# Kernel tuning notes

Measured on AMD Instinct MI355X. Metric: run time of the kernel, lower is better.

Reference implementation:

```python
import jax, jax.numpy as jnp
import numpy as np

NUM_LANDMARKS = 64
INV_ITERS = 6
B, S, D = 32, 8192, 64  # batch*heads, seq_len, head_dim


def landmark_pool(x, n=NUM_LANDMARKS):
    # x: [B, S, D]; S % n == 0 -> mean over contiguous segments of length S//n
    b, s, d = x.shape
    seg = s // n
    return x.reshape(b, n, seg, d).mean(axis=2)  # [B, n, D]


def iterative_pinv(k_mat, n_iter=INV_ITERS):
    # k_mat: [B, m, m] row-stochastic softmax matrix; Razavi Newton-Schulz pinv
    m = k_mat.shape[-1]
    i_mat = jnp.eye(m, dtype=k_mat.dtype)
    # per-batch init: 1 / max_j(sum_i K_ij) * K^T
    col_sums = jnp.sum(k_mat, axis=-2)                      # [B, m]
    init_scale = 1.0 / jnp.max(col_sums, axis=-1)           # [B]
    v = init_scale[:, None, None] * jnp.swapaxes(k_mat, -1, -2)
    for _ in range(n_iter):
        kv = jnp.matmul(k_mat, v)
        v = jnp.matmul(0.25 * v, 13.0 * i_mat - jnp.matmul(kv, 15.0 * i_mat - jnp.matmul(kv, 7.0 * i_mat - kv)))
    return v


def setup_inputs() -> dict:
    key = jax.random.key(0)
    kq, kk, kv = jax.random.split(key, 3)
    q = jax.random.normal(kq, (B, S, D), dtype=jnp.float32)
    k = jax.random.normal(kk, (B, S, D), dtype=jnp.float32)
    v = jax.random.normal(kv, (B, S, D), dtype=jnp.float32)
    return {"q": q, "k": k, "v": v}


def reference(q, k, v):
    d = k.shape[-1]
    scale = 1.0 / jnp.sqrt(jnp.asarray(d, dtype=q.dtype))
    q_land = landmark_pool(q)   # [B, m, D]
    k_land = landmark_pool(k)   # [B, m, D]
    # kernel_1: softmax(q k_land^T / sqrt(d))  -> [B, S, m]
    kernel_1 = jax.nn.softmax(jnp.einsum('bsd,bmd->bsm', q * scale, k_land), axis=-1)
    # kernel_2: softmax(q_land k_land^T / sqrt(d)) -> [B, m, m]
    kernel_2 = jax.nn.softmax(jnp.einsum('bnd,bmd->bnm', q_land * scale, k_land), axis=-1)
    # kernel_3: softmax(q_land k^T / sqrt(d)) @ v -> [B, m, D]
    att_3 = jax.nn.softmax(jnp.einsum('bmd,bsd->bms', q_land * scale, k), axis=-1)
    kernel_3 = jnp.einsum('bms,bsd->bmd', att_3, v)
    kernel_2_inv = iterative_pinv(kernel_2)
    x = jnp.einsum('bsm,bmn->bsn', kernel_1, kernel_2_inv)
    x = jnp.einsum('bsn,bnd->bsd', x, kernel_3)
    return x
```

## Files before the change

### kernel.cpp

```cpp
#include <hip/hip_runtime.h>
#include <math.h>

#define NB 32
#define SLEN 8192
#define DIM 64
#define M 64
#define SEG 128
#define SPLITS 32
#define CHUNK 256


#define ACC16(ax0, ax1, ax2, ax3, bv)                                          \
  c[0][0] = fmaf(ax0, bv.x, c[0][0]); c[0][1] = fmaf(ax0, bv.y, c[0][1]);      \
  c[0][2] = fmaf(ax0, bv.z, c[0][2]); c[0][3] = fmaf(ax0, bv.w, c[0][3]);      \
  c[1][0] = fmaf(ax1, bv.x, c[1][0]); c[1][1] = fmaf(ax1, bv.y, c[1][1]);      \
  c[1][2] = fmaf(ax1, bv.z, c[1][2]); c[1][3] = fmaf(ax1, bv.w, c[1][3]);      \
  c[2][0] = fmaf(ax2, bv.x, c[2][0]); c[2][1] = fmaf(ax2, bv.y, c[2][1]);      \
  c[2][2] = fmaf(ax2, bv.z, c[2][2]); c[2][3] = fmaf(ax2, bv.w, c[2][3]);      \
  c[3][0] = fmaf(ax3, bv.x, c[3][0]); c[3][1] = fmaf(ax3, bv.y, c[3][1]);      \
  c[3][2] = fmaf(ax3, bv.z, c[3][2]); c[3][3] = fmaf(ax3, bv.w, c[3][3]);

__device__ __forceinline__ void mm_p1(const float* A, int lda, const float* B,
                                      int ldb, int r0, int n0, float (&c)[4][4]) {
  #pragma unroll 4
  for (int kk = 0; kk < 64; kk += 4) {
    float4 a0 = *(const float4*)(A + (r0 + 0) * lda + kk);
    float4 a1 = *(const float4*)(A + (r0 + 1) * lda + kk);
    float4 a2 = *(const float4*)(A + (r0 + 2) * lda + kk);
    float4 a3 = *(const float4*)(A + (r0 + 3) * lda + kk);
    float4 b0 = *(const float4*)(B + (kk + 0) * ldb + n0);
    float4 b1 = *(const float4*)(B + (kk + 1) * ldb + n0);
    float4 b2 = *(const float4*)(B + (kk + 2) * ldb + n0);
    float4 b3 = *(const float4*)(B + (kk + 3) * ldb + n0);
    ACC16(a0.x, a1.x, a2.x, a3.x, b0)
    ACC16(a0.y, a1.y, a2.y, a3.y, b1)
    ACC16(a0.z, a1.z, a2.z, a3.z, b2)
    ACC16(a0.w, a1.w, a2.w, a3.w, b3)
  }
}

__device__ __forceinline__ void mm_p1_tf(const float* A, int lda, const float* B,
                                         int ldb, float cd, int r0, int n0,
                                         float (&c)[4][4]) {
  #pragma unroll 4
  for (int kk = 0; kk < 64; kk += 4) {
    float4 a0 = *(const float4*)(A + (r0 + 0) * lda + kk);
    float4 a1 = *(const float4*)(A + (r0 + 1) * lda + kk);
    float4 a2 = *(const float4*)(A + (r0 + 2) * lda + kk);
    float4 a3 = *(const float4*)(A + (r0 + 3) * lda + kk);
    #pragma unroll
    for (int t = 0; t < 4; ++t) {
      float4 bb = *(const float4*)(B + (kk + t) * ldb + n0);
      int r = kk + t;
      bb.x = ((r == n0 + 0) ? cd : 0.f) - bb.x;
      bb.y = ((r == n0 + 1) ? cd : 0.f) - bb.y;
      bb.z = ((r == n0 + 2) ? cd : 0.f) - bb.z;
      bb.w = ((r == n0 + 3) ? cd : 0.f) - bb.w;
      float av0 = (t == 0) ? a0.x : (t == 1) ? a0.y : (t == 2) ? a0.z : a0.w;
      float av1 = (t == 0) ? a1.x : (t == 1) ? a1.y : (t == 2) ? a1.z : a1.w;
      float av2 = (t == 0) ? a2.x : (t == 1) ? a2.y : (t == 2) ? a2.z : a2.w;
      float av3 = (t == 0) ? a3.x : (t == 1) ? a3.y : (t == 2) ? a3.z : a3.w;
      ACC16(av0, av1, av2, av3, bb)
    }
  }
}

__device__ __forceinline__ void mm_p2(const float* A, int lda, const float* B,
                                      int ldb, int m0, int n0, float (&c)[4][4]) {
  #pragma unroll 4
  for (int s = 0; s < 64; ++s) {
    float4 e = *(const float4*)(A + s * lda + m0);
    float4 vv = *(const float4*)(B + s * ldb + n0);
    ACC16(e.x, e.y, e.z, e.w, vv)
  }
}

__global__ __launch_bounds__(256) void pool_kernel(
    const float* __restrict__ q, const float* __restrict__ k,
    float* __restrict__ ql_s, float* __restrict__ kl) {
  int b = blockIdx.x >> 6, n = blockIdx.x & 63;
  int tid = threadIdx.x;
  int rg = tid >> 4, d4 = tid & 15;
  const float* qb = q + ((size_t)b * SLEN + (size_t)n * SEG) * DIM;
  const float* kb = k + ((size_t)b * SLEN + (size_t)n * SEG) * DIM;
  float4 aq = make_float4(0.f, 0.f, 0.f, 0.f);
  float4 ak = make_float4(0.f, 0.f, 0.f, 0.f);
  #pragma unroll
  for (int j = 0; j < 8; ++j) {
    int r = rg * 8 + j;
    float4 t = *(const float4*)(qb + r * DIM + 4 * d4);
    aq.x += t.x; aq.y += t.y; aq.z += t.z; aq.w += t.w;
    float4 u = *(const float4*)(kb + r * DIM + 4 * d4);
    ak.x += u.x; ak.y += u.y; ak.z += u.z; ak.w += u.w;
  }
  __shared__ float4 sq[256], sk[256];
  sq[tid] = aq; sk[tid] = ak;
  __syncthreads();
  #pragma unroll
  for (int off = 128; off >= 16; off >>= 1) {
    if (tid < off) {
      float4 a = sq[tid], bb = sq[tid + off];
      sq[tid] = make_float4(a.x + bb.x, a.y + bb.y, a.z + bb.z, a.w + bb.w);
      float4 c2 = sk[tid], d2 = sk[tid + off];
      sk[tid] = make_float4(c2.x + d2.x, c2.y + d2.y, c2.z + d2.z, c2.w + d2.w);
    }
    __syncthreads();
  }
  if (tid < 16) {
    float4 a = sq[tid], bb = sk[tid];
    size_t o = ((size_t)b * M + n) * DIM + 4 * tid;
    const float qs = 0.125f / 128.f, ks = 1.f / 128.f;
    *(float4*)(ql_s + o) = make_float4(a.x * qs, a.y * qs, a.z * qs, a.w * qs);
    *(float4*)(kl + o) = make_float4(bb.x * ks, bb.y * ks, bb.z * ks, bb.w * ks);
  }
}

__global__ __launch_bounds__(256) void phaseB_pinv_kernel(
    const float* __restrict__ k, const float* __restrict__ v,
    const float* __restrict__ ql_s, const float* __restrict__ klg,
    float* num_p, float* den_p, float* k2inv_g, float* k2_g) {
  __shared__ float smem[13312];
  int tid = threadIdx.x;
  int r0 = (tid >> 4) << 2, c0 = (tid & 15) << 2;

  if (blockIdx.x >= NB) {
    int blk = blockIdx.x - NB;
    int b = blk >> 5, sp = blk & 31;
    float* qlT = smem;
    float* kv = smem + 4352;
    float* Es = smem + 8704;
    float* dredF = smem + 13056;

    #pragma unroll
    for (int i = 0; i < 16; ++i) {
      int e = tid + 256 * i;
      qlT[(e & 63) * 68 + (e >> 6)] = ql_s[(size_t)b * 4096 + e];
    }
    int m_den = tid & 63, qg = tid >> 6;
    float den_acc = 0.f;
    float cN[4][4];
    #pragma unroll
    for (int i = 0; i < 4; ++i)
      #pragma unroll
      for (int j = 0; j < 4; ++j) cN[i][j] = 0.f;

    const float* kbase = k + ((size_t)b * SLEN + (size_t)sp * CHUNK) * DIM;
    const float* vbase = v + ((size_t)b * SLEN + (size_t)sp * CHUNK) * DIM;

    for (int sc = 0; sc < 4; ++sc) {
      #pragma unroll
      for (int i = 0; i < 4; ++i) {
        int idx = tid + 256 * i;
        int s = idx >> 4, j = idx & 15;
        *(float4*)(kv + s * 68 + 4 * j) =
            *(const float4*)(kbase + (size_t)(sc * 64 + s) * DIM + 4 * j);
      }
      __syncthreads();
      float c[4][4];
      #pragma unroll
      for (int i = 0; i < 4; ++i)
        #pragma unroll
        for (int j = 0; j < 4; ++j) c[i][j] = 0.f;
      mm_p1(kv, 68, qlT, 68, r0, c0, c);
      #pragma unroll
      for (int i = 0; i < 4; ++i)
        #pragma unroll
        for (int j = 0; j < 4; ++j) c[i][j] = __expf(c[i][j]);
      __syncthreads();
      #pragma unroll
      for (int i = 0; i < 4; ++i)
        *(float4*)(Es + (r0 + i) * 68 + c0) =
            make_float4(c[i][0], c[i][1], c[i][2], c[i][3]);
      #pragma unroll
      for (int i = 0; i < 4; ++i) {
        int idx = tid + 256 * i;
        int s = idx >> 4, j = idx & 15;
        *(float4*)(kv + s * 68 + 4 * j) =
            *(const float4*)(vbase + (size_t)(sc * 64 + s) * DIM + 4 * j);
      }
      __syncthreads();
      #pragma unroll
      for (int t = 0; t < 16; ++t) den_acc += Es[(qg * 16 + t) * 68 + m_den];
      mm_p2(Es, 68, kv, 68, r0, c0, cN);
      __syncthreads();
    }
    dredF[qg * 64 + m_den] = den_acc;
    __syncthreads();
    if (tid < 64)
      den_p[((size_t)b * SPLITS + sp) * 64 + tid] =
          dredF[tid] + dredF[64 + tid] + dredF[128 + tid] + dredF[192 + tid];
    float* np = num_p + ((size_t)b * SPLITS + sp) * 4096;
    #pragma unroll
    for (int i = 0; i < 4; ++i)
      *(float4*)(np + (size_t)(r0 + i) * 64 + c0) =
          make_float4(cN[i][0], cN[i][1], cN[i][2], cN[i][3]);
  } else {
    int b = blockIdx.x;
    float* b1 = smem;
    float* b2 = smem + 4352;
    float* b3 = smem + 8704;
    float* red = smem + 13056;
    float* k2b = k2_g + (size_t)b * 4096;

    #pragma unroll
    for (int i = 0; i < 4; ++i) {
      int idx = tid + 256 * i;
      int s = idx >> 4, j = idx & 15;
      *(float4*)(b1 + s * 68 + 4 * j) =
          *(const float4*)(ql_s + (size_t)b * 4096 + (size_t)s * 64 + 4 * j);
    }
    #pragma unroll
    for (int i = 0; i < 16; ++i) {
      int e = tid + 256 * i;
      b2[(e & 63) * 68 + (e >> 6)] = klg[(size_t)b * 4096 + e];
    }
    __syncthreads();
    float c[4][4];
    #pragma unroll
    for (int i = 0; i < 4; ++i)
      #pragma unroll
      for (int j = 0; j < 4; ++j) c[i][j] = 0.f;
    mm_p1(b1, 68, b2, 68, r0, c0, c);
    #pragma unroll
    for (int i = 0; i < 4; ++i) {
      float pr = 0.f;
      #pragma unroll
      for (int j = 0; j < 4; ++j) { c[i][j] = __expf(c[i][j]); pr += c[i][j]; }
      b3[(r0 + i) * 16 + (tid & 15)] = pr;
    }
    __syncthreads();
    if (tid < 64) {
      float rs = 0.f;
      #pragma unroll
      for (int g = 0; g < 16; ++g) rs += b3[tid * 16 + g];
      red[tid] = 1.f / rs;
    }
    __syncthreads();
    #pragma unroll
    for (int i = 0; i < 4; ++i) {
      float inv = red[r0 + i];
      #pragma unroll
      for (int j = 0; j < 4; ++j) c[i][j] *= inv;
      float4 val = make_float4(c[i][0], c[i][1], c[i][2], c[i][3]);
      *(float4*)(k2b + (size_t)(r0 + i) * 64 + c0) = val;
      *(float4*)(b3 + (r0 + i) * 68 + c0) = val;
    }
    __syncthreads();
    if (tid < 64) {
      float cs = 0.f;
      #pragma unroll 8
      for (int n2 = 0; n2 < 64; ++n2) cs += b3[n2 * 68 + tid];
      float mx = cs;
      #pragma unroll
      for (int off = 1; off < 64; off <<= 1) mx = fmaxf(mx, __shfl_xor(mx, off));
      red[0] = 1.f / mx;
    }
    __syncthreads();
    float iscale = red[0];
    #pragma unroll
    for (int i = 0; i < 16; ++i) {
      int e = tid + 256 * i;
      int r = e >> 6, cc = e & 63;
      b1[r * 68 + cc] = b3[cc * 68 + r] * iscale;
    }
    __syncthreads();

    for (int it = 0; it < 6; ++it) {
      #pragma unroll
      for (int i = 0; i < 4; ++i)
        #pragma unroll
        for (int j = 0; j < 4; ++j) c[i][j] = 0.f;
      mm_p1(k2b, 64, b1, 68, r0, c0, c);
      #pragma unroll
      for (int i = 0; i < 4; ++i)
        *(float4*)(b2 + (r0 + i) * 68 + c0) =
            make_float4(c[i][0], c[i][1], c[i][2], c[i][3]);
      __syncthreads();
      #pragma unroll
      for (int i = 0; i < 4; ++i)
        #pragma unroll
        for (int j = 0; j < 4; ++j) c[i][j] = 0.f;
      mm_p1_tf(b2, 68, b2, 68, 7.f, r0, c0, c);
      #pragma unroll
      for (int i = 0; i < 4; ++i)
        *(float4*)(b3 + (r0 + i) * 68 + c0) =
            make_float4(c[i][0], c[i][1], c[i][2], c[i][3]);
      __syncthreads();
      #pragma unroll
      for (int i = 0; i < 4; ++i)
        #pragma unroll
        for (int j = 0; j < 4; ++j) c[i][j] = 0.f;
      mm_p1_tf(b2, 68, b3, 68, 15.f, r0, c0, c);
      __syncthreads();
      #pragma unroll
      for (int i = 0; i < 4; ++i)
        *(float4*)(b3 + (r0 + i) * 68 + c0) =
            make_float4(c[i][0], c[i][1], c[i][2], c[i][3]);
      __syncthreads();
      #pragma unroll
      for (int i = 0; i < 4; ++i)
        #pragma unroll
        for (int j = 0; j < 4; ++j) c[i][j] = 0.f;
      mm_p1_tf(b1, 68, b3, 68, 13.f, r0, c0, c);
      __syncthreads();
      #pragma unroll
      for (int i = 0; i < 4; ++i)
        *(float4*)(b1 + (r0 + i) * 68 + c0) = make_float4(
            0.25f * c[i][0], 0.25f * c[i][1], 0.25f * c[i][2], 0.25f * c[i][3]);
      __syncthreads();
    }
    #pragma unroll
    for (int i = 0; i < 16; ++i) {
      int e = tid + 256 * i;
      k2inv_g[(size_t)b * 4096 + e] = b1[(e >> 6) * 68 + (e & 63)];
    }
  }
}

__global__ __launch_bounds__(256) void combine1_kernel(
    const float* __restrict__ num_p, const float* __restrict__ den_p,
    float* __restrict__ k3) {
  int b = blockIdx.x >> 3, slice = blockIdx.x & 7;
  int tid = threadIdx.x;
  int e0 = slice * 512 + tid * 2;
  float a0 = 0.f, a1 = 0.f;
  for (int sp = 0; sp < SPLITS; ++sp) {
    float2 t = *(const float2*)(num_p + ((size_t)b * SPLITS + sp) * 4096 + e0);
    a0 += t.x; a1 += t.y;
  }
  int m = e0 >> 6;
  float dsum = 0.f;
  for (int sp = 0; sp < SPLITS; ++sp)
    dsum += den_p[((size_t)b * SPLITS + sp) * 64 + m];
  float dinv = 1.f / dsum;
  *(float2*)(k3 + (size_t)b * 4096 + e0) = make_float2(a0 * dinv, a1 * dinv);
}

__global__ __launch_bounds__(256) void combine2_kernel(
    const float* __restrict__ k2inv, const float* __restrict__ k3,
    float* __restrict__ Wm) {
  __shared__ float A[4352], Bm[4352];
  int b = blockIdx.x, tid = threadIdx.x;
  int r0 = (tid >> 4) << 2, c0 = (tid & 15) << 2;
  #pragma unroll
  for (int i = 0; i < 4; ++i) {
    int idx = tid + 256 * i;
    int s = idx >> 4, j = idx & 15;
    *(float4*)(A + s * 68 + 4 * j) =
        *(const float4*)(k2inv + (size_t)b * 4096 + (size_t)s * 64 + 4 * j);
    *(float4*)(Bm + s * 68 + 4 * j) =
        *(const float4*)(k3 + (size_t)b * 4096 + (size_t)s * 64 + 4 * j);
  }
  __syncthreads();
  float c[4][4];
  #pragma unroll
  for (int i = 0; i < 4; ++i)
    #pragma unroll
    for (int j = 0; j < 4; ++j) c[i][j] = 0.f;
  mm_p1(A, 68, Bm, 68, r0, c0, c);
  #pragma unroll
  for (int i = 0; i < 4; ++i)
    *(float4*)(Wm + (size_t)b * 4096 + (size_t)(r0 + i) * 64 + c0) =
        make_float4(c[i][0], c[i][1], c[i][2], c[i][3]);
}

#define FROWS 128
__global__ __launch_bounds__(256) void final_kernel(
    const float* __restrict__ q, const float* __restrict__ klg,
    const float* __restrict__ Wm, float* __restrict__ out) {
  __shared__ float smem[13120];
  float* klT = smem;
  float* Wl = smem + 4352;
  float* Es = smem + 8448;
  float* dred = smem + 12800;
  float* denF = smem + 13056;
  int b = blockIdx.x >> 6, rb = blockIdx.x & 63;
  int tid = threadIdx.x;
  int r0 = (tid >> 4) << 2, c0 = (tid & 15) << 2;
  int rr = tid & 63, qg = tid >> 6;

  #pragma unroll
  for (int i = 0; i < 16; ++i) {
    int e = tid + 256 * i;
    klT[(e & 63) * 68 + (e >> 6)] = klg[(size_t)b * 4096 + e];
  }
  #pragma unroll
  for (int i = 0; i < 4; ++i) {
    int idx = tid + 256 * i;
    *(float4*)(Wl + idx * 4) = *(const float4*)(Wm + (size_t)b * 4096 + idx * 4);
  }
  __syncthreads();

  for (int sc = 0; sc < FROWS / 64; ++sc) {
    const float* qsrc = q + ((size_t)b * SLEN + (size_t)rb * FROWS + sc * 64) * DIM;
    #pragma unroll
    for (int i = 0; i < 4; ++i) {
      int idx = tid + 256 * i;
      int s = idx >> 4, j = idx & 15;
      float4 t = *(const float4*)(qsrc + (size_t)s * DIM + 4 * j);
      *(float4*)(Es + s * 68 + 4 * j) =
          make_float4(t.x * 0.125f, t.y * 0.125f, t.z * 0.125f, t.w * 0.125f);
    }
    __syncthreads();
    float c[4][4];
    #pragma unroll
    for (int i = 0; i < 4; ++i)
      #pragma unroll
      for (int j = 0; j < 4; ++j) c[i][j] = 0.f;
    mm_p1(Es, 68, klT, 68, r0, c0, c);
    #pragma unroll
    for (int i = 0; i < 4; ++i)
      #pragma unroll
      for (int j = 0; j < 4; ++j) c[i][j] = __expf(c[i][j]);
    __syncthreads();
    #pragma unroll
    for (int i = 0; i < 4; ++i)
      *(float4*)(Es + (r0 + i) * 68 + c0) =
          make_float4(c[i][0], c[i][1], c[i][2], c[i][3]);
    __syncthreads();
    float ds = 0.f;
    #pragma unroll
    for (int t = 0; t < 4; ++t) {
      float4 x = *(const float4*)(Es + rr * 68 + qg * 16 + 4 * t);
      ds += (x.x + x.y) + (x.z + x.w);
    }
    dred[qg * 64 + rr] = ds;
    __syncthreads();
    if (tid < 64)
      denF[tid] =
          1.f / (dred[tid] + dred[64 + tid] + dred[128 + tid] + dred[192 + tid]);
    __syncthreads();
    float c3[4][4];
    #pragma unroll
    for (int i = 0; i < 4; ++i)
      #pragma unroll
      for (int j = 0; j < 4; ++j) c3[i][j] = 0.f;
    mm_p1(Es, 68, Wl, 64, r0, c0, c3);
    float* orow = out + ((size_t)b * SLEN + (size_t)rb * FROWS + sc * 64) * DIM;
    #pragma unroll
    for (int i = 0; i < 4; ++i) {
      float inv = denF[r0 + i];
      *(float4*)(orow + (size_t)(r0 + i) * 64 + c0) = make_float4(
          c3[i][0] * inv, c3[i][1] * inv, c3[i][2] * inv, c3[i][3] * inv);
    }
    __syncthreads();
  }
}

extern "C" void kernel_launch(void* const* d_in, const int* in_sizes, int n_in,
                              void* d_out, int out_size, void* d_ws, size_t ws_size,
                              hipStream_t stream) {
  (void)in_sizes; (void)n_in; (void)out_size; (void)ws_size;
  const float* q = (const float*)d_in[0];
  const float* k = (const float*)d_in[1];
  const float* v = (const float*)d_in[2];
  float* out = (float*)d_out;
  float* ws = (float*)d_ws;

  float* ql_s = ws;
  float* kl = ws + 131072;
  float* k2inv = ws + 262144;
  float* Wm = ws + 393216;
  float* k3 = ws + 524288;
  float* den_p = ws + 655360;
  float* num_p = ws + 720896;

  pool_kernel<<<NB * 64, 256, 0, stream>>>(q, k, ql_s, kl);
  phaseB_pinv_kernel<<<NB + NB * SPLITS, 256, 0, stream>>>(
      k, v, ql_s, kl, num_p, den_p, k2inv, Wm);
  combine1_kernel<<<NB * 8, 256, 0, stream>>>(num_p, den_p, k3);
  combine2_kernel<<<NB, 256, 0, stream>>>(k2inv, k3, Wm);
  final_kernel<<<NB * 64, 256, 0, stream>>>(q, kl, Wm, out);
}
```

Before: 350.1 us.

## Prefetch tiles into registers, enlarge per-block chunks, shuffle-reduce softmax denominators

The phase-B and final kernels now load the next 64-row tile of k/v or q into registers while the current tile is computed, so global load latency overlaps with the LDS matmuls. Each block handles more rows (chunk 512, 16 splits; final kernel 512 rows per block), which cuts the block count and the redundant per-block setup of landmark and weight tiles. The final kernel computes row-sum denominators with 16-lane shuffles instead of an LDS reduction, removing two barriers per tile. The cost is fewer blocks in flight on a large GPU, extra register pressure from the prefetch buffers, and dependence on combine1 honouring the new SPLITS value.

Measured after the change: 367.3 us. 1.05x slower.

```diff
diff --git a/kernel.cpp b/kernel.cpp
--- a/kernel.cpp
+++ b/kernel.cpp
@@ -6,8 +6,11 @@
 #define DIM 64
 #define M 64
 #define SEG 128
-#define SPLITS 32
-#define CHUNK 256
+#define SPLITS 16
+#define CHUNK 512
+#define TILES 8
+#define FROWS 512
+#define FTILES 8
 
 
 #define ACC16(ax0, ax1, ax2, ax3, bv)                                          \
@@ -75,6 +78,19 @@
   }
 }
 
+__device__ __forceinline__ void load_tile4(float4 (&dst)[4], const float* base,
+                                           int t, int srow, int scol4) {
+  #pragma unroll
+  for (int i = 0; i < 4; ++i)
+    dst[i] = *(const float4*)(base + (size_t)(t * 64 + srow + 16 * i) * DIM + scol4);
+}
+__device__ __forceinline__ void store_tile4(float* lds, const float4 (&src)[4],
+                                            int srow, int scol4) {
+  #pragma unroll
+  for (int i = 0; i < 4; ++i)
+    *(float4*)(lds + (srow + 16 * i) * 68 + scol4) = src[i];
+}
+
 __global__ __launch_bounds__(256) void pool_kernel(
     const float* __restrict__ q, const float* __restrict__ k,
     float* __restrict__ ql_s, float* __restrict__ kl) {
@@ -122,10 +138,11 @@
   __shared__ float smem[13312];
   int tid = threadIdx.x;
   int r0 = (tid >> 4) << 2, c0 = (tid & 15) << 2;
+  int srow = tid >> 4, scol4 = (tid & 15) << 2;
 
   if (blockIdx.x >= NB) {
     int blk = blockIdx.x - NB;
-    int b = blk >> 5, sp = blk & 31;
+    int b = blk >> 4, sp = blk & 15;
     float* qlT = smem;
     float* kv = smem + 4352;
     float* Es = smem + 8704;
@@ -147,14 +164,13 @@
     const float* kbase = k + ((size_t)b * SLEN + (size_t)sp * CHUNK) * DIM;
     const float* vbase = v + ((size_t)b * SLEN + (size_t)sp * CHUNK) * DIM;
 
-    for (int sc = 0; sc < 4; ++sc) {
-      #pragma unroll
-      for (int i = 0; i < 4; ++i) {
-        int idx = tid + 256 * i;
-        int s = idx >> 4, j = idx & 15;
-        *(float4*)(kv + s * 68 + 4 * j) =
-            *(const float4*)(kbase + (size_t)(sc * 64 + s) * DIM + 4 * j);
-      }
+    float4 kreg[4], vreg[4];
+    load_tile4(kreg, kbase, 0, srow, scol4);
+    load_tile4(vreg, vbase, 0, srow, scol4);
+
+    for (int sc = 0; sc < TILES; ++sc) {
+      store_tile4(kv, kreg, srow, scol4);
+      if (sc < TILES - 1) load_tile4(kreg, kbase, sc + 1, srow, scol4);
       __syncthreads();
       float c[4][4];
       #pragma unroll
@@ -167,17 +183,12 @@
         #pragma unroll
         for (int j = 0; j < 4; ++j) c[i][j] = __expf(c[i][j]);
       __syncthreads();
+      store_tile4(kv, vreg, srow, scol4);
       #pragma unroll
       for (int i = 0; i < 4; ++i)
         *(float4*)(Es + (r0 + i) * 68 + c0) =
             make_float4(c[i][0], c[i][1], c[i][2], c[i][3]);
-      #pragma unroll
-      for (int i = 0; i < 4; ++i) {
-        int idx = tid + 256 * i;
-        int s = idx >> 4, j = idx & 15;
-        *(float4*)(kv + s * 68 + 4 * j) =
-            *(const float4*)(vbase + (size_t)(sc * 64 + s) * DIM + 4 * j);
-      }
+      if (sc < TILES - 1) load_tile4(vreg, vbase, sc + 1, srow, scol4);
       __syncthreads();
       #pragma unroll
       for (int t = 0; t < 16; ++t) den_acc += Es[(qg * 16 + t) * 68 + m_den];
@@ -364,20 +375,17 @@
         make_float4(c[i][0], c[i][1], c[i][2], c[i][3]);
 }
 
-#define FROWS 128
 __global__ __launch_bounds__(256) void final_kernel(
     const float* __restrict__ q, const float* __restrict__ klg,
     const float* __restrict__ Wm, float* __restrict__ out) {
-  __shared__ float smem[13120];
+  __shared__ float smem[12800];
   float* klT = smem;
   float* Wl = smem + 4352;
   float* Es = smem + 8448;
-  float* dred = smem + 12800;
-  float* denF = smem + 13056;
-  int b = blockIdx.x >> 6, rb = blockIdx.x & 63;
+  int b = blockIdx.x >> 4, rb = blockIdx.x & 15;
   int tid = threadIdx.x;
   int r0 = (tid >> 4) << 2, c0 = (tid & 15) << 2;
-  int rr = tid & 63, qg = tid >> 6;
+  int srow = tid >> 4, scol4 = (tid & 15) << 2;
 
   #pragma unroll
   for (int i = 0; i < 16; ++i) {
@@ -389,18 +397,20 @@
     int idx = tid + 256 * i;
     *(float4*)(Wl + idx * 4) = *(const float4*)(Wm + (size_t)b * 4096 + idx * 4);
   }
-  __syncthreads();
-
-  for (int sc = 0; sc < FROWS / 64; ++sc) {
-    const float* qsrc = q + ((size_t)b * SLEN + (size_t)rb * FROWS + sc * 64) * DIM;
+
+  const float* qbase = q + ((size_t)b * SLEN + (size_t)rb * FROWS) * DIM;
+  float* obase = out + ((size_t)b * SLEN + (size_t)rb * FROWS) * DIM;
+  float4 qreg[4];
+  load_tile4(qreg, qbase, 0, srow, scol4);
+
+  for (int sc = 0; sc < FTILES; ++sc) {
     #pragma unroll
     for (int i = 0; i < 4; ++i) {
-      int idx = tid + 256 * i;
-      int s = idx >> 4, j = idx & 15;
-      float4 t = *(const float4*)(qsrc + (size_t)s * DIM + 4 * j);
-      *(float4*)(Es + s * 68 + 4 * j) =
+      float4 t = qreg[i];
+      *(float4*)(Es + (srow + 16 * i) * 68 + scol4) =
           make_float4(t.x * 0.125f, t.y * 0.125f, t.z * 0.125f, t.w * 0.125f);
     }
+    if (sc < FTILES - 1) load_tile4(qreg, qbase, sc + 1, srow, scol4);
     __syncthreads();
     float c[4][4];
     #pragma unroll
@@ -412,37 +422,31 @@
     for (int i = 0; i < 4; ++i)
       #pragma unroll
       for (int j = 0; j < 4; ++j) c[i][j] = __expf(c[i][j]);
-    __syncthreads();
+    float inv[4];
+    #pragma unroll
+    for (int i = 0; i < 4; ++i) {
+      float s = (c[i][0] + c[i][1]) + (c[i][2] + c[i][3]);
+      s += __shfl_xor(s, 1);
+      s += __shfl_xor(s, 2);
+      s += __shfl_xor(s, 4);
+      s += __shfl_xor(s, 8);
+      inv[i] = 1.f / s;
+    }
     #pragma unroll
     for (int i = 0; i < 4; ++i)
       *(float4*)(Es + (r0 + i) * 68 + c0) =
           make_float4(c[i][0], c[i][1], c[i][2], c[i][3]);
-    __syncthreads();
-    float ds = 0.f;
-    #pragma unroll
-    for (int t = 0; t < 4; ++t) {
-      float4 x = *(const float4*)(Es + rr * 68 + qg * 16 + 4 * t);
-      ds += (x.x + x.y) + (x.z + x.w);
-    }
-    dred[qg * 64 + rr] = ds;
-    __syncthreads();
-    if (tid < 64)
-      denF[tid] =
-          1.f / (dred[tid] + dred[64 + tid] + dred[128 + tid] + dred[192 + tid]);
-    __syncthreads();
     float c3[4][4];
     #pragma unroll
     for (int i = 0; i < 4; ++i)
       #pragma unroll
       for (int j = 0; j < 4; ++j) c3[i][j] = 0.f;
     mm_p1(Es, 68, Wl, 64, r0, c0, c3);
-    float* orow = out + ((size_t)b * SLEN + (size_t)rb * FROWS + sc * 64) * DIM;
-    #pragma unroll
-    for (int i = 0; i < 4; ++i) {
-      float inv = denF[r0 + i];
-      *(float4*)(orow + (size_t)(r0 + i) * 64 + c0) = make_float4(
-          c3[i][0] * inv, c3[i][1] * inv, c3[i][2] * inv, c3[i][3] * inv);
-    }
+    #pragma unroll
+    for (int i = 0; i < 4; ++i)
+      *(float4*)(obase + (size_t)(sc * 64 + r0 + i) * 64 + c0) = make_float4(
+          c3[i][0] * inv[i], c3[i][1] * inv[i], c3[i][2] * inv[i],
+          c3[i][3] * inv[i]);
     __syncthreads();
   }
 }
@@ -470,5 +474,5 @@
       k, v, ql_s, kl, num_p, den_p, k2inv, Wm);
   combine1_kernel<<<NB * 8, 256, 0, stream>>>(num_p, den_p, k3);
   combine2_kernel<<<NB, 256, 0, stream>>>(k2inv, k3, Wm);
-  final_kernel<<<NB * 64, 256, 0, stream>>>(q, kl, Wm, out);
-}
+  final_kernel<<<NB * 16, 256, 0, stream>>>(q, kl, Wm, out);
+}
```
